# Kernel optimization log

Measured on AMD Instinct MI355X. Metric: run time of the kernel, lower is better.

Reference implementation:

```python
import jax, jax.numpy as jnp
import numpy as np

B, L, F = 16, 1024, 64
D = 256          # d_model (expand_factor=1 -> d_inner == d_model)
S = 2            # num_scales
N = 16           # state_size
H = 32           # fc hidden
EPS = 1e-5


def setup_inputs() -> dict:
    key = jax.random.key(0)
    ks = jax.random.split(key, 20)
    g = lambda i, shape, s=0.05: jax.random.normal(ks[i], shape, dtype=jnp.float32) * s
    return {
        "x": jax.random.normal(ks[0], (B, L, F), dtype=jnp.float32),
        "W_in": g(1, (F, D)), "b_in": jnp.zeros((D,), jnp.float32),
        # per-scale liquid-Mamba params, stacked over scales
        "Wd": g(2, (S, D, D)), "bd": jnp.zeros((S, D), jnp.float32),
        "WB": g(3, (S, D, N)), "WC": g(4, (S, D, N)),
        "Wtau": g(5, (S, D, D)),
        "A_log": jnp.broadcast_to(jnp.log(jnp.arange(1, N + 1, dtype=jnp.float32)), (S, D, N)).copy(),
        "Dp": jnp.ones((S, D), jnp.float32),
        "Wout": g(6, (S, D, D)),
        # head
        "ln_g": jnp.ones((D,), jnp.float32), "ln_b": jnp.zeros((D,), jnp.float32),
        "W1": g(7, (D, H)), "b1": jnp.zeros((H,), jnp.float32),
        "W2": g(8, (H, 1)), "b2": jnp.zeros((1,), jnp.float32),
    }


def _liquid_ssm(x, Wd, bd, WB, WC, Wtau, A_log, Dp, Wout):
    # x: [B,L,D] -> y: [B,L,D]. Selective scan with liquid time-constant gate.
    delta = jax.nn.softplus(jnp.einsum('bld,de->ble', x, Wd) + bd)   # [B,L,D]
    tau = jax.nn.sigmoid(jnp.einsum('bld,de->ble', x, Wtau))          # liquid gate
    delta = delta * tau
    Bm = jnp.einsum('bld,dn->bln', x, WB)                             # [B,L,N]
    Cm = jnp.einsum('bld,dn->bln', x, WC)                             # [B,L,N]
    A = -jnp.exp(A_log)                                               # [D,N]
    dA = jnp.exp(delta[..., None] * A)                                # [B,L,D,N]
    dBx = delta[..., None] * Bm[:, :, None, :] * x[..., None]         # [B,L,D,N]

    def step(h, inp):
        a_t, bx_t, c_t = inp                                          # [B,D,N],[B,D,N],[B,N]
        h = a_t * h + bx_t
        y = jnp.einsum('bdn,bn->bd', h, c_t)
        return h, y

    h0 = jnp.zeros((x.shape[0], x.shape[2], A.shape[1]), x.dtype)
    _, ys = jax.lax.scan(step, h0,
                         (dA.transpose(1, 0, 2, 3), dBx.transpose(1, 0, 2, 3), Cm.transpose(1, 0, 2)))
    y = ys.transpose(1, 0, 2) + x * Dp                                # skip connection
    return jnp.einsum('bld,de->ble', y, Wout)


def reference(x, W_in, b_in, Wd, bd, WB, WC, Wtau, A_log, Dp, Wout,
              ln_g, ln_b, W1, b1, W2, b2):
    h = jnp.einsum('blf,fd->bld', x, W_in) + b_in                     # input projection
    outs = [_liquid_ssm(h, Wd[s], bd[s], WB[s], WC[s], Wtau[s], A_log[s], Dp[s], Wout[s])
            for s in range(Wd.shape[0])]
    mamba_out = sum(outs) / len(outs)                                 # average over scales
    last = mamba_out[:, -1, :]                                        # [B,D]
    mu = jnp.mean(last, axis=-1, keepdims=True)
    var = jnp.var(last, axis=-1, keepdims=True)
    z = (last - mu) * jax.lax.rsqrt(var + EPS) * ln_g + ln_b          # LayerNorm
    z = jax.nn.relu(z @ W1 + b1)                                      # dropout is identity in eval
    return z @ W2 + b2                                                # [B,1]
```

## Files before the change

kernel.cpp:

```cpp
#include <hip/hip_runtime.h>
#include <hip/hip_bf16.h>
#include <math.h>

#define B_   16
#define L_   1024
#define F_   64
#define D_   256
#define S_   2
#define N_   16
#define H_   32
#define EPS_ 1e-5f
#define BL_  (B_*L_)
#define NCH_ 8
#define TC_  (L_/NCH_)
#define SUB_ 64
#define TSTR_ 68
#define LOG2E_ 1.44269504088896340736f
#define XBLK_ (BL_*F_/1024)

typedef __attribute__((ext_vector_type(8))) short  bf16x8;
typedef __attribute__((ext_vector_type(4))) float  f32x4;
typedef __attribute__((ext_vector_type(2))) float  f32x2;

typedef const __attribute__((address_space(1))) void* gas_ptr;
typedef __attribute__((address_space(3))) void*       las_ptr;

#if defined(__has_builtin)
# if __has_builtin(__builtin_amdgcn_exp2f)
#  define EXP2(x) __builtin_amdgcn_exp2f(x)
#  define ASCALE_ LOG2E_
# endif
#endif
#ifndef EXP2
# define EXP2(x) __expf(x)
# define ASCALE_ 1.0f
#endif

__device__ inline void async_copy16(const void* g, void* l) {
    __builtin_amdgcn_global_load_lds((gas_ptr)g, (las_ptr)l, 16, 0, 0);
}

__device__ inline unsigned short f2bf_rne(float x) {
    union { float f; unsigned u; } v; v.f = x;
    unsigned r = v.u + 0x7fff + ((v.u >> 16) & 1);
    return (unsigned short)(r >> 16);
}

__global__ __launch_bounds__(256) void k_prep(const float* __restrict__ x,
                                              const float* __restrict__ Win,
                                              const float* __restrict__ bin,
                                              const float* __restrict__ Wd,
                                              const float* __restrict__ bd,
                                              const float* __restrict__ Wt,
                                              const float* __restrict__ WB,
                                              unsigned short* __restrict__ x_hi,
                                              unsigned short* __restrict__ Weff_hi,
                                              float* __restrict__ bias_eff,
                                              unsigned short* __restrict__ WinT_hi,
                                              unsigned short* __restrict__ WBe_hi,
                                              float* __restrict__ bbias)
{
    const int blk = blockIdx.x;
    const int tid = threadIdx.x;

    if (blk < XBLK_) {
        const int i = (blk * 256 + tid) * 4;
        float4 v = *(const float4*)(x + i);
        ushort4 h4;
        h4.x = f2bf_rne(v.x);
        h4.y = f2bf_rne(v.y);
        h4.z = f2bf_rne(v.z);
        h4.w = f2bf_rne(v.w);
        *(ushort4*)(x_hi + i) = h4;
        return;
    }

    const int job4 = blk - XBLK_;
    const int j    = tid >> 6;
    const int f    = tid & 63;
    const int job  = job4 * 4 + j;

    __shared__ float col[4][D_];

    if (job < 1024) {
        const int s = job >> 9, n = job & 511;
        const float* W = (n < 256) ? (Wd + (size_t)s * D_ * D_) : (Wt + (size_t)s * D_ * D_);
        const int e = n & 255;
        for (int d = f; d < D_; d += 64) col[j][d] = W[(size_t)d * D_ + e];
        __syncthreads();
        float a = 0.f;
        for (int d = 0; d < D_; ++d) a += Win[(size_t)f * D_ + d] * col[j][d];
        Weff_hi[((size_t)s * 512 + n) * F_ + f] = f2bf_rne(a);
        if (f == 0) {
            float bb = 0.f;
            for (int d = 0; d < D_; ++d) bb += bin[d] * col[j][d];
            if (n < 256) bb += bd[s * D_ + e];
            bias_eff[s * 512 + n] = bb;
        }
    } else if (job < 1024 + D_) {
        const int d = job - 1024;
        WinT_hi[(size_t)d * F_ + f] = f2bf_rne(Win[(size_t)f * D_ + d]);
    } else {
        const int idx = job - (1024 + D_);
        const int s = idx >> 4, n = idx & 15;
        const float* wb = WB + (size_t)s * D_ * N_;
        float a = 0.f;
        for (int d = 0; d < D_; ++d) a += Win[(size_t)f * D_ + d] * wb[(size_t)d * N_ + n];
        WBe_hi[((size_t)s * N_ + n) * F_ + f] = f2bf_rne(a);
        if (f == 0) {
            float bb = 0.f;
            for (int d = 0; d < D_; ++d) bb += bin[d] * wb[(size_t)d * N_ + n];
            bbias[s * N_ + n] = bb;
        }
    }
}

__global__ __launch_bounds__(256) void k_fused_scan(
        const unsigned short* __restrict__ x_hi,
        const unsigned short* __restrict__ Weff_hi,
        const unsigned short* __restrict__ WinT_hi,
        const unsigned short* __restrict__ WBe_hi,
        const float* __restrict__ bias_eff,
        const float* __restrict__ bin,
        const float* __restrict__ bbias,
        const float* __restrict__ A_log,
        float* __restrict__ part,
        float* __restrict__ csum)
{
    const int dtile = blockIdx.x >> 3;
    const int c     = blockIdx.x & 7;
    const int b     = blockIdx.y;
    const int s     = blockIdx.z;
    const int d0    = dtile * 16;
    const int tid   = threadIdx.x;
    const int wid   = tid >> 6;
    const int lane  = tid & 63;
    const int l15   = lane & 15;
    const int quad  = lane >> 4;
    const int dl    = tid & 15;
    const int nl    = tid >> 4;

    __shared__ unsigned short Wh[64 * F_];
    __shared__ float sdl[16][TSTR_];
    __shared__ float sq [16][TSTR_];
    __shared__ float sb [16][TSTR_];

    const int r8 = lane >> 3;
    const int c8 = lane & 7;

    #pragma unroll
    for (int call = 0; call < 2; ++call) {
        const int rr = call * 8 + r8;
        const int ar = wid * 16 + rr;
        const int lc = (c8 - ar) & 7;
        const unsigned short* gh;
        if (wid == 0)      gh = Weff_hi + ((size_t)s * 512 + d0 + rr) * F_ + lc * 8;
        else if (wid == 1) gh = Weff_hi + ((size_t)s * 512 + 256 + d0 + rr) * F_ + lc * 8;
        else if (wid == 2) gh = WinT_hi + ((size_t)(d0 + rr)) * F_ + lc * 8;
        else               gh = WBe_hi + ((size_t)s * N_ + rr) * F_ + lc * 8;
        async_copy16(gh, &Wh[(wid * 16 + call * 8) * F_]);
    }

    const float bias_d = bias_eff[s * 512 + d0 + l15];
    const float bias_t = bias_eff[s * 512 + 256 + d0 + l15];
    const float bin_v  = bin[d0 + l15];
    const float bb_v   = bbias[s * N_ + l15];
    const float A2 = -__expf(A_log[((size_t)s * D_ + d0 + dl) * N_ + nl]) * ASCALE_;

    f32x2 st01 = {0.f, 0.f};
    f32x2 st23 = {0.f, 0.f};
    float As = 0.f;

    const int qoff = quad * 8;
    const int nsc  = TC_ / SUB_;

    bf16x8 fah0, fah1;
    {
        const size_t rowb = ((size_t)b * L_ + c * TC_ + (nsc - 1) * SUB_ + wid * 16 + l15) * F_;
        fah0 = *(const bf16x8*)(x_hi + rowb + qoff);
        fah1 = *(const bf16x8*)(x_hi + rowb + 32 + qoff);
    }
    __syncthreads();

    for (int sc = nsc - 1; sc >= 0; --sc) {
        f32x4 acc[4];
        #pragma unroll
        for (int g = 0; g < 4; ++g) acc[g] = (f32x4){0.f, 0.f, 0.f, 0.f};
        #pragma unroll
        for (int ks = 0; ks < 2; ++ks) {
            bf16x8 ah = ks ? fah1 : fah0;
            #pragma unroll
            for (int g = 0; g < 4; ++g) {
                const int brow = g * 16 + l15;
                const int pcB  = ((ks * 4 + quad) + brow) & 7;
                bf16x8 bh = *(const bf16x8*)&Wh[brow * F_ + pcB * 8];
                acc[g] = __builtin_amdgcn_mfma_f32_16x16x32_bf16(ah, bh, acc[g], 0, 0, 0);
            }
        }

        bf16x8 nah0, nah1;
        const bool more = (sc > 0);
        if (more) {
            const size_t rowb = ((size_t)b * L_ + c * TC_ + (sc - 1) * SUB_ + wid * 16 + l15) * F_;
            nah0 = *(const bf16x8*)(x_hi + rowb + qoff);
            nah1 = *(const bf16x8*)(x_hi + rowb + 32 + qoff);
        }

        __syncthreads();

        {
            f32x4 wd_, wq_, wb_;
            #pragma unroll
            for (int r = 0; r < 4; ++r) {
                const float pd  = acc[0][r] + bias_d;
                const float sp  = fmaxf(pd, 0.f) + __logf(1.f + __expf(-fabsf(pd)));
                const float sg  = 1.f / (1.f + __expf(-(acc[1][r] + bias_t)));
                const float dlt = sp * sg;
                const float hv  = acc[2][r] + bin_v;
                wd_[r] = dlt;
                wq_[r] = dlt * hv;
                wb_[r] = acc[3][r] + bb_v;
            }
            const int tcol = wid * 16 + quad * 4;
            *(f32x4*)&sdl[l15][tcol] = wd_;
            *(f32x4*)&sq [l15][tcol] = wq_;
            *(f32x4*)&sb [l15][tcol] = wb_;
        }
        __syncthreads();

        #pragma unroll 4
        for (int tt = SUB_ - 4; tt >= 0; tt -= 4) {
            f32x4 dp = *(const f32x4*)&sdl[dl][tt];
            f32x4 qp = *(const f32x4*)&sq [dl][tt];
            f32x4 bp = *(const f32x4*)&sb [nl][tt];
            const float a2v = fmaf(A2, dp.w, As);
            const float a1v = fmaf(A2, dp.z, a2v);
            const float a0v = fmaf(A2, dp.y, a1v);
            f32x2 e01, e23;
            e23.y = EXP2(As);
            e23.x = EXP2(a2v);
            e01.y = EXP2(a1v);
            e01.x = EXP2(a0v);
            f32x2 q01 = {qp.x, qp.y}, q23 = {qp.z, qp.w};
            f32x2 b01 = {bp.x, bp.y}, b23 = {bp.z, bp.w};
            st01 = q01 * b01 * e01 + st01;
            st23 = q23 * b23 * e23 + st23;
            As = fmaf(A2, dp.x, a0v);
        }

        if (more) { fah0 = nah0; fah1 = nah1; }
    }

    const size_t pb = ((size_t)s * B_ + b) * NCH_ + c;
    part[(pb * D_ + d0 + dl) * N_ + nl] = (st01.x + st01.y) + (st23.x + st23.y);
    if (nl == 0)
        csum[pb * D_ + d0 + dl] = As / A2;
}

__global__ __launch_bounds__(256) void k_ys(const float* __restrict__ x,
                                            const float* __restrict__ Win,
                                            const float* __restrict__ bin,
                                            const float* __restrict__ part,
                                            const float* __restrict__ csum,
                                            const float* __restrict__ A_log,
                                            const float* __restrict__ WC,
                                            const float* __restrict__ Dp,
                                            float* __restrict__ ys)
{
    const int s   = blockIdx.x;
    const int b   = blockIdx.y;
    const int tid = threadIdx.x;

    __shared__ float xr[F_];
    __shared__ float hl[D_];
    __shared__ float cm[N_];
    __shared__ float cred[N_][17];

    if (tid < F_) xr[tid] = x[((size_t)b * L_ + (L_ - 1)) * F_ + tid];
    __syncthreads();

    {
        float a = bin[tid];
        for (int f = 0; f < F_; ++f) a += xr[f] * Win[(size_t)f * D_ + tid];
        hl[tid] = a;
    }
    __syncthreads();

    {
        const int n  = tid & 15;
        const int dq = tid >> 4;
        float a = 0.f;
        for (int d = dq * 16; d < dq * 16 + 16; ++d)
            a += hl[d] * WC[((size_t)s * D_ + d) * N_ + n];
        cred[n][dq] = a;
    }
    __syncthreads();
    if (tid < N_) {
        float a = 0.f;
        #pragma unroll
        for (int q = 0; q < 16; ++q) a += cred[tid][q];
        cm[tid] = a;
    }
    __syncthreads();

    const float* al = A_log + ((size_t)s * D_ + tid) * N_;
    float a2v[N_];
    #pragma unroll
    for (int n = 0; n < N_; ++n) a2v[n] = -__expf(al[n]);
    const size_t cbase = ((size_t)s * B_ + b) * NCH_;
    float acc = 0.f;
    float tail = 0.f;
    for (int c = NCH_ - 1; c >= 0; --c) {
        const float* pp = part + ((cbase + c) * D_ + tid) * N_;
        #pragma unroll
        for (int n = 0; n < N_; ++n)
            acc += cm[n] * __expf(a2v[n] * tail) * pp[n];
        tail += csum[(cbase + c) * D_ + tid];
    }
    ys[((size_t)s * B_ + b) * D_ + tid] = acc + hl[tid] * Dp[s * D_ + tid];
}

__global__ __launch_bounds__(256) void k_last(const float* __restrict__ ys,
                                              const float* __restrict__ Wout,
                                              float* __restrict__ last)
{
    const int b  = blockIdx.x;
    const int e0 = blockIdx.y * 64;
    const int tid = threadIdx.x;
    const int e  = tid & 63;
    const int kq = tid >> 6;

    __shared__ float ysl[S_ * D_];
    __shared__ float red[4][64];

    #pragma unroll
    for (int j = tid; j < S_ * D_; j += 256) {
        const int ss = j >> 8, dd = j & 255;
        ysl[j] = ys[((size_t)ss * B_ + b) * D_ + dd];
    }
    __syncthreads();

    float a = 0.f;
    for (int k = kq * 128; k < kq * 128 + 128; ++k) {
        const int ss = k >> 8, dd = k & 255;
        a += ysl[k] * Wout[((size_t)ss * D_ + dd) * D_ + e0 + e];
    }
    red[kq][e] = a;
    __syncthreads();
    if (kq == 0) {
        const float v = (red[0][e] + red[1][e] + red[2][e] + red[3][e]) * (1.f / S_);
        last[(size_t)b * D_ + e0 + e] = v;
    }
}

__global__ __launch_bounds__(256) void k_head(const float* __restrict__ last,
                                              const float* __restrict__ ln_g,
                                              const float* __restrict__ ln_b,
                                              const float* __restrict__ W1,
                                              const float* __restrict__ b1,
                                              const float* __restrict__ W2,
                                              const float* __restrict__ b2,
                                              float* __restrict__ out)
{
    const int b   = blockIdx.x;
    const int tid = threadIdx.x;

    __shared__ float zv[D_];
    __shared__ float red1[256];
    __shared__ float red2[256];
    __shared__ float r1[H_];

    const float v = last[(size_t)b * D_ + tid];
    red1[tid] = v;
    red2[tid] = v * v;
    __syncthreads();
    for (int off = 128; off > 0; off >>= 1) {
        if (tid < off) { red1[tid] += red1[tid + off]; red2[tid] += red2[tid + off]; }
        __syncthreads();
    }
    const float mu  = red1[0] * (1.f / D_);
    const float var = red2[0] * (1.f / D_) - mu * mu;
    const float z = (v - mu) * rsqrtf(var + EPS_) * ln_g[tid] + ln_b[tid];
    zv[tid] = z;
    __syncthreads();

    if (tid < H_) {
        float a = b1[tid];
        for (int e = 0; e < D_; ++e) a += zv[e] * W1[(size_t)e * H_ + tid];
        r1[tid] = fmaxf(a, 0.f);
    }
    __syncthreads();
    if (tid == 0) {
        float a = b2[0];
        for (int j = 0; j < H_; ++j) a += r1[j] * W2[j];
        out[b] = a;
    }
}

extern "C" void kernel_launch(void* const* d_in, const int* in_sizes, int n_in,
                              void* d_out, int out_size, void* d_ws, size_t ws_size,
                              hipStream_t stream)
{
    const float* x     = (const float*)d_in[0];
    const float* Win   = (const float*)d_in[1];
    const float* bin   = (const float*)d_in[2];
    const float* Wd    = (const float*)d_in[3];
    const float* bd    = (const float*)d_in[4];
    const float* WB    = (const float*)d_in[5];
    const float* WC    = (const float*)d_in[6];
    const float* Wtau  = (const float*)d_in[7];
    const float* A_log = (const float*)d_in[8];
    const float* Dp    = (const float*)d_in[9];
    const float* Wout  = (const float*)d_in[10];
    const float* ln_g  = (const float*)d_in[11];
    const float* ln_b  = (const float*)d_in[12];
    const float* W1    = (const float*)d_in[13];
    const float* b1    = (const float*)d_in[14];
    const float* W2    = (const float*)d_in[15];
    const float* b2    = (const float*)d_in[16];
    float* out = (float*)d_out;

    char* ws = (char*)d_ws;
    const size_t MB = 1024 * 1024;
    const size_t KB = 1024;
    unsigned short* x_hi     = (unsigned short*)(ws);
    unsigned short* Weff_hi  = (unsigned short*)(ws + 2 * MB);
    unsigned short* WinT_hi  = (unsigned short*)(ws + 2 * MB + 128 * KB);
    unsigned short* WBe_hi   = (unsigned short*)(ws + 2 * MB + 160 * KB);
    float*          bias_eff = (float*)(ws + 2 * MB + 164 * KB);
    float*          bbias    = (float*)(ws + 2 * MB + 168 * KB);
    float*          part     = (float*)(ws + 3 * MB);
    float*          csum     = (float*)(ws + 7 * MB);
    float*          ysbuf    = (float*)(ws + 7 * MB + 256 * KB);
    float*          lastbuf  = (float*)(ws + 7 * MB + 288 * KB);

    hipLaunchKernelGGL(k_prep, dim3(XBLK_ + 328), dim3(256), 0, stream,
                       x, Win, bin, Wd, bd, Wtau, WB,
                       x_hi, Weff_hi, bias_eff, WinT_hi, WBe_hi, bbias);
    hipLaunchKernelGGL(k_fused_scan, dim3((D_ / 16) * NCH_, B_, S_), dim3(256), 0, stream,
                       x_hi, Weff_hi, WinT_hi, WBe_hi,
                       bias_eff, bin, bbias, A_log, part, csum);
    hipLaunchKernelGGL(k_ys,   dim3(S_, B_), dim3(256), 0, stream,
                       x, Win, bin, part, csum, A_log, WC, Dp, ysbuf);
    hipLaunchKernelGGL(k_last, dim3(B_, 4), dim3(256), 0, stream, ysbuf, Wout, lastbuf);
    hipLaunchKernelGGL(k_head, dim3(B_), dim3(256), 0, stream,
                       lastbuf, ln_g, ln_b, W1, b1, W2, b2, out);
}
```

Baseline: 162.1 us.

## Double scan chunks to one tile each and fuse tail kernels into one

Doubles the number of sequence chunks in the fused scan so each block handles a single 64-step tile, dropping the inner sub-chunk loop, the prefetch and one barrier per tile while launching twice as many blocks. The three small epilogue kernels (chunk combine, output projection, head) are merged into a single per-batch kernel to remove two launches and their intermediate global buffers. The cost is twice the partial-state traffic and a longer serial chunk combine, and the fused tail runs on only 16 blocks, each doing the full Wout matvec serially per thread.

```diff
diff --git a/kernel.cpp b/kernel.cpp
--- a/kernel.cpp
+++ b/kernel.cpp
@@ -11,9 +11,8 @@
 #define H_   32
 #define EPS_ 1e-5f
 #define BL_  (B_*L_)
-#define NCH_ 8
+#define NCH_ 16
 #define TC_  (L_/NCH_)
-#define SUB_ 64
 #define TSTR_ 68
 #define LOG2E_ 1.44269504088896340736f
 #define XBLK_ (BL_*F_/1024)
@@ -127,8 +126,8 @@
         float* __restrict__ part,
         float* __restrict__ csum)
 {
-    const int dtile = blockIdx.x >> 3;
-    const int c     = blockIdx.x & 7;
+    const int dtile = blockIdx.x >> 4;
+    const int c     = blockIdx.x & 15;
     const int b     = blockIdx.y;
     const int s     = blockIdx.z;
     const int d0    = dtile * 16;
@@ -167,88 +166,71 @@
     const float bb_v   = bbias[s * N_ + l15];
     const float A2 = -__expf(A_log[((size_t)s * D_ + d0 + dl) * N_ + nl]) * ASCALE_;
 
+    const int qoff = quad * 8;
+    bf16x8 fah0, fah1;
+    {
+        const size_t rowb = ((size_t)b * L_ + c * TC_ + wid * 16 + l15) * F_;
+        fah0 = *(const bf16x8*)(x_hi + rowb + qoff);
+        fah1 = *(const bf16x8*)(x_hi + rowb + 32 + qoff);
+    }
+    __syncthreads();
+
+    f32x4 acc[4];
+    #pragma unroll
+    for (int g = 0; g < 4; ++g) acc[g] = (f32x4){0.f, 0.f, 0.f, 0.f};
+    #pragma unroll
+    for (int ks = 0; ks < 2; ++ks) {
+        bf16x8 ah = ks ? fah1 : fah0;
+        #pragma unroll
+        for (int g = 0; g < 4; ++g) {
+            const int brow = g * 16 + l15;
+            const int pcB  = ((ks * 4 + quad) + brow) & 7;
+            bf16x8 bh = *(const bf16x8*)&Wh[brow * F_ + pcB * 8];
+            acc[g] = __builtin_amdgcn_mfma_f32_16x16x32_bf16(ah, bh, acc[g], 0, 0, 0);
+        }
+    }
+
+    {
+        f32x4 wd_, wq_, wb_;
+        #pragma unroll
+        for (int r = 0; r < 4; ++r) {
+            const float pd  = acc[0][r] + bias_d;
+            const float sp  = fmaxf(pd, 0.f) + __logf(1.f + __expf(-fabsf(pd)));
+            const float sg  = 1.f / (1.f + __expf(-(acc[1][r] + bias_t)));
+            const float dlt = sp * sg;
+            const float hv  = acc[2][r] + bin_v;
+            wd_[r] = dlt;
+            wq_[r] = dlt * hv;
+            wb_[r] = acc[3][r] + bb_v;
+        }
+        const int tcol = wid * 16 + quad * 4;
+        *(f32x4*)&sdl[l15][tcol] = wd_;
+        *(f32x4*)&sq [l15][tcol] = wq_;
+        *(f32x4*)&sb [l15][tcol] = wb_;
+    }
+    __syncthreads();
+
     f32x2 st01 = {0.f, 0.f};
     f32x2 st23 = {0.f, 0.f};
     float As = 0.f;
-
-    const int qoff = quad * 8;
-    const int nsc  = TC_ / SUB_;
-
-    bf16x8 fah0, fah1;
-    {
-        const size_t rowb = ((size_t)b * L_ + c * TC_ + (nsc - 1) * SUB_ + wid * 16 + l15) * F_;
-        fah0 = *(const bf16x8*)(x_hi + rowb + qoff);
-        fah1 = *(const bf16x8*)(x_hi + rowb + 32 + qoff);
-    }
-    __syncthreads();
-
-    for (int sc = nsc - 1; sc >= 0; --sc) {
-        f32x4 acc[4];
-        #pragma unroll
-        for (int g = 0; g < 4; ++g) acc[g] = (f32x4){0.f, 0.f, 0.f, 0.f};
-        #pragma unroll
-        for (int ks = 0; ks < 2; ++ks) {
-            bf16x8 ah = ks ? fah1 : fah0;
-            #pragma unroll
-            for (int g = 0; g < 4; ++g) {
-                const int brow = g * 16 + l15;
-                const int pcB  = ((ks * 4 + quad) + brow) & 7;
-                bf16x8 bh = *(const bf16x8*)&Wh[brow * F_ + pcB * 8];
-                acc[g] = __builtin_amdgcn_mfma_f32_16x16x32_bf16(ah, bh, acc[g], 0, 0, 0);
-            }
-        }
-
-        bf16x8 nah0, nah1;
-        const bool more = (sc > 0);
-        if (more) {
-            const size_t rowb = ((size_t)b * L_ + c * TC_ + (sc - 1) * SUB_ + wid * 16 + l15) * F_;
-            nah0 = *(const bf16x8*)(x_hi + rowb + qoff);
-            nah1 = *(const bf16x8*)(x_hi + rowb + 32 + qoff);
-        }
-
-        __syncthreads();
-
-        {
-            f32x4 wd_, wq_, wb_;
-            #pragma unroll
-            for (int r = 0; r < 4; ++r) {
-                const float pd  = acc[0][r] + bias_d;
-                const float sp  = fmaxf(pd, 0.f) + __logf(1.f + __expf(-fabsf(pd)));
-                const float sg  = 1.f / (1.f + __expf(-(acc[1][r] + bias_t)));
-                const float dlt = sp * sg;
-                const float hv  = acc[2][r] + bin_v;
-                wd_[r] = dlt;
-                wq_[r] = dlt * hv;
-                wb_[r] = acc[3][r] + bb_v;
-            }
-            const int tcol = wid * 16 + quad * 4;
-            *(f32x4*)&sdl[l15][tcol] = wd_;
-            *(f32x4*)&sq [l15][tcol] = wq_;
-            *(f32x4*)&sb [l15][tcol] = wb_;
-        }
-        __syncthreads();
-
-        #pragma unroll 4
-        for (int tt = SUB_ - 4; tt >= 0; tt -= 4) {
-            f32x4 dp = *(const f32x4*)&sdl[dl][tt];
-            f32x4 qp = *(const f32x4*)&sq [dl][tt];
-            f32x4 bp = *(const f32x4*)&sb [nl][tt];
-            const float a2v = fmaf(A2, dp.w, As);
-            const float a1v = fmaf(A2, dp.z, a2v);
-            const float a0v = fmaf(A2, dp.y, a1v);
-            f32x2 e01, e23;
-            e23.y = EXP2(As);
-            e23.x = EXP2(a2v);
-            e01.y = EXP2(a1v);
-            e01.x = EXP2(a0v);
-            f32x2 q01 = {qp.x, qp.y}, q23 = {qp.z, qp.w};
-            f32x2 b01 = {bp.x, bp.y}, b23 = {bp.z, bp.w};
-            st01 = q01 * b01 * e01 + st01;
-            st23 = q23 * b23 * e23 + st23;
-            As = fmaf(A2, dp.x, a0v);
-        }
-
-        if (more) { fah0 = nah0; fah1 = nah1; }
+    #pragma unroll 4
+    for (int tt = TC_ - 4; tt >= 0; tt -= 4) {
+        f32x4 dp = *(const f32x4*)&sdl[dl][tt];
+        f32x4 qp = *(const f32x4*)&sq [dl][tt];
+        f32x4 bp = *(const f32x4*)&sb [nl][tt];
+        const float a2v = fmaf(A2, dp.w, As);
+        const float a1v = fmaf(A2, dp.z, a2v);
+        const float a0v = fmaf(A2, dp.y, a1v);
+        f32x2 e01, e23;
+        e23.y = EXP2(As);
+        e23.x = EXP2(a2v);
+        e01.y = EXP2(a1v);
+        e01.x = EXP2(a0v);
+        f32x2 q01 = {qp.x, qp.y}, q23 = {qp.z, qp.w};
+        f32x2 b01 = {bp.x, bp.y}, b23 = {bp.z, bp.w};
+        st01 = q01 * b01 * e01 + st01;
+        st23 = q23 * b23 * e23 + st23;
+        As = fmaf(A2, dp.x, a0v);
     }
 
     const size_t pb = ((size_t)s * B_ + b) * NCH_ + c;
@@ -257,103 +239,15 @@
         csum[pb * D_ + d0 + dl] = As / A2;
 }
 
-__global__ __launch_bounds__(256) void k_ys(const float* __restrict__ x,
-                                            const float* __restrict__ Win,
-                                            const float* __restrict__ bin,
-                                            const float* __restrict__ part,
-                                            const float* __restrict__ csum,
-                                            const float* __restrict__ A_log,
-                                            const float* __restrict__ WC,
-                                            const float* __restrict__ Dp,
-                                            float* __restrict__ ys)
-{
-    const int s   = blockIdx.x;
-    const int b   = blockIdx.y;
-    const int tid = threadIdx.x;
-
-    __shared__ float xr[F_];
-    __shared__ float hl[D_];
-    __shared__ float cm[N_];
-    __shared__ float cred[N_][17];
-
-    if (tid < F_) xr[tid] = x[((size_t)b * L_ + (L_ - 1)) * F_ + tid];
-    __syncthreads();
-
-    {
-        float a = bin[tid];
-        for (int f = 0; f < F_; ++f) a += xr[f] * Win[(size_t)f * D_ + tid];
-        hl[tid] = a;
-    }
-    __syncthreads();
-
-    {
-        const int n  = tid & 15;
-        const int dq = tid >> 4;
-        float a = 0.f;
-        for (int d = dq * 16; d < dq * 16 + 16; ++d)
-            a += hl[d] * WC[((size_t)s * D_ + d) * N_ + n];
-        cred[n][dq] = a;
-    }
-    __syncthreads();
-    if (tid < N_) {
-        float a = 0.f;
-        #pragma unroll
-        for (int q = 0; q < 16; ++q) a += cred[tid][q];
-        cm[tid] = a;
-    }
-    __syncthreads();
-
-    const float* al = A_log + ((size_t)s * D_ + tid) * N_;
-    float a2v[N_];
-    #pragma unroll
-    for (int n = 0; n < N_; ++n) a2v[n] = -__expf(al[n]);
-    const size_t cbase = ((size_t)s * B_ + b) * NCH_;
-    float acc = 0.f;
-    float tail = 0.f;
-    for (int c = NCH_ - 1; c >= 0; --c) {
-        const float* pp = part + ((cbase + c) * D_ + tid) * N_;
-        #pragma unroll
-        for (int n = 0; n < N_; ++n)
-            acc += cm[n] * __expf(a2v[n] * tail) * pp[n];
-        tail += csum[(cbase + c) * D_ + tid];
-    }
-    ys[((size_t)s * B_ + b) * D_ + tid] = acc + hl[tid] * Dp[s * D_ + tid];
-}
-
-__global__ __launch_bounds__(256) void k_last(const float* __restrict__ ys,
+__global__ __launch_bounds__(256) void k_tail(const float* __restrict__ x,
+                                              const float* __restrict__ Win,
+                                              const float* __restrict__ bin,
+                                              const float* __restrict__ part,
+                                              const float* __restrict__ csum,
+                                              const float* __restrict__ A_log,
+                                              const float* __restrict__ WC,
+                                              const float* __restrict__ Dp,
                                               const float* __restrict__ Wout,
-                                              float* __restrict__ last)
-{
-    const int b  = blockIdx.x;
-    const int e0 = blockIdx.y * 64;
-    const int tid = threadIdx.x;
-    const int e  = tid & 63;
-    const int kq = tid >> 6;
-
-    __shared__ float ysl[S_ * D_];
-    __shared__ float red[4][64];
-
-    #pragma unroll
-    for (int j = tid; j < S_ * D_; j += 256) {
-        const int ss = j >> 8, dd = j & 255;
-        ysl[j] = ys[((size_t)ss * B_ + b) * D_ + dd];
-    }
-    __syncthreads();
-
-    float a = 0.f;
-    for (int k = kq * 128; k < kq * 128 + 128; ++k) {
-        const int ss = k >> 8, dd = k & 255;
-        a += ysl[k] * Wout[((size_t)ss * D_ + dd) * D_ + e0 + e];
-    }
-    red[kq][e] = a;
-    __syncthreads();
-    if (kq == 0) {
-        const float v = (red[0][e] + red[1][e] + red[2][e] + red[3][e]) * (1.f / S_);
-        last[(size_t)b * D_ + e0 + e] = v;
-    }
-}
-
-__global__ __launch_bounds__(256) void k_head(const float* __restrict__ last,
                                               const float* __restrict__ ln_g,
                                               const float* __restrict__ ln_b,
                                               const float* __restrict__ W1,
@@ -365,12 +259,73 @@
     const int b   = blockIdx.x;
     const int tid = threadIdx.x;
 
+    __shared__ float xr[F_];
+    __shared__ float hl[D_];
+    __shared__ float cm[S_][N_];
+    __shared__ float cred[N_][17];
+    __shared__ float ysl[S_][D_];
     __shared__ float zv[D_];
     __shared__ float red1[256];
     __shared__ float red2[256];
     __shared__ float r1[H_];
 
-    const float v = last[(size_t)b * D_ + tid];
+    if (tid < F_) xr[tid] = x[((size_t)b * L_ + (L_ - 1)) * F_ + tid];
+    __syncthreads();
+
+    {
+        float a = bin[tid];
+        for (int f = 0; f < F_; ++f) a += xr[f] * Win[(size_t)f * D_ + tid];
+        hl[tid] = a;
+    }
+    __syncthreads();
+
+    for (int s = 0; s < S_; ++s) {
+        const int n  = tid & 15;
+        const int dq = tid >> 4;
+        float a = 0.f;
+        for (int d = dq * 16; d < dq * 16 + 16; ++d)
+            a += hl[d] * WC[((size_t)s * D_ + d) * N_ + n];
+        cred[n][dq] = a;
+        __syncthreads();
+        if (tid < N_) {
+            float acc = 0.f;
+            #pragma unroll
+            for (int q = 0; q < 16; ++q) acc += cred[tid][q];
+            cm[s][tid] = acc;
+        }
+        __syncthreads();
+    }
+
+    for (int s = 0; s < S_; ++s) {
+        const float* al = A_log + ((size_t)s * D_ + tid) * N_;
+        float a2v[N_];
+        #pragma unroll
+        for (int n = 0; n < N_; ++n) a2v[n] = -__expf(al[n]);
+        const size_t cbase = ((size_t)s * B_ + b) * NCH_;
+        float acc = 0.f;
+        float tail = 0.f;
+        for (int c = NCH_ - 1; c >= 0; --c) {
+            const float* pp = part + ((cbase + c) * D_ + tid) * N_;
+            #pragma unroll
+            for (int n = 0; n < N_; ++n)
+                acc += cm[s][n] * __expf(a2v[n] * tail) * pp[n];
+            tail += csum[(cbase + c) * D_ + tid];
+        }
+        ysl[s][tid] = acc + hl[tid] * Dp[s * D_ + tid];
+    }
+    __syncthreads();
+
+    float v;
+    {
+        float a = 0.f;
+        #pragma unroll 2
+        for (int s = 0; s < S_; ++s) {
+            const float* wo = Wout + (size_t)s * D_ * D_;
+            for (int d = 0; d < D_; ++d) a += ysl[s][d] * wo[(size_t)d * D_ + tid];
+        }
+        v = a * (1.f / S_);
+    }
+
     red1[tid] = v;
     red2[tid] = v * v;
     __syncthreads();
@@ -430,9 +385,7 @@
     float*          bias_eff = (float*)(ws + 2 * MB + 164 * KB);
     float*          bbias    = (float*)(ws + 2 * MB + 168 * KB);
     float*          part     = (float*)(ws + 3 * MB);
-    float*          csum     = (float*)(ws + 7 * MB);
-    float*          ysbuf    = (float*)(ws + 7 * MB + 256 * KB);
-    float*          lastbuf  = (float*)(ws + 7 * MB + 288 * KB);
+    float*          csum     = (float*)(ws + 11 * MB);
 
     hipLaunchKernelGGL(k_prep, dim3(XBLK_ + 328), dim3(256), 0, stream,
                        x, Win, bin, Wd, bd, Wtau, WB,
@@ -440,9 +393,7 @@
     hipLaunchKernelGGL(k_fused_scan, dim3((D_ / 16) * NCH_, B_, S_), dim3(256), 0, stream,
                        x_hi, Weff_hi, WinT_hi, WBe_hi,
                        bias_eff, bin, bbias, A_log, part, csum);
-    hipLaunchKernelGGL(k_ys,   dim3(S_, B_), dim3(256), 0, stream,
-                       x, Win, bin, part, csum, A_log, WC, Dp, ysbuf);
-    hipLaunchKernelGGL(k_last, dim3(B_, 4), dim3(256), 0, stream, ysbuf, Wout, lastbuf);
-    hipLaunchKernelGGL(k_head, dim3(B_), dim3(256), 0, stream,
-                       lastbuf, ln_g, ln_b, W1, b1, W2, b2, out);
-}
+    hipLaunchKernelGGL(k_tail, dim3(B_), dim3(256), 0, stream,
+                       x, Win, bin, part, csum, A_log, WC, Dp, Wout,
+                       ln_g, ln_b, W1, b1, W2, b2, out);
+}
```

New measurement: 180.0 us. 1.11x slower.

## Double scan chunk count and parallelize chunk combine over d-tiles

Applied to the files above, without the earlier changes.

Splits the sequence into 16 chunks of 64 steps instead of 8 chunks of 128, so each scan block does one MFMA projection and one 64-step scan with no inner sub-chunk loop or prefetch. This doubles the grid of the fused scan kernel (more blocks to fill the CUs, shorter serial chain per block). The combine kernel k_ys is re-gridded over 16-wide d tiles, with each thread handling one (d,n) pair plus a shared-memory reduction, so the longer chunk carry runs in parallel. The cost is twice the partial-state traffic, and the combine kernel now recomputes its input projection in every d-tile block.

```diff
diff --git a/kernel.cpp b/kernel.cpp
--- a/kernel.cpp
+++ b/kernel.cpp
@@ -11,9 +11,8 @@
 #define H_   32
 #define EPS_ 1e-5f
 #define BL_  (B_*L_)
-#define NCH_ 8
+#define NCH_ 16
 #define TC_  (L_/NCH_)
-#define SUB_ 64
 #define TSTR_ 68
 #define LOG2E_ 1.44269504088896340736f
 #define XBLK_ (BL_*F_/1024)
@@ -127,8 +126,8 @@
         float* __restrict__ part,
         float* __restrict__ csum)
 {
-    const int dtile = blockIdx.x >> 3;
-    const int c     = blockIdx.x & 7;
+    const int dtile = blockIdx.x >> 4;
+    const int c     = blockIdx.x & 15;
     const int b     = blockIdx.y;
     const int s     = blockIdx.z;
     const int d0    = dtile * 16;
@@ -167,88 +166,71 @@
     const float bb_v   = bbias[s * N_ + l15];
     const float A2 = -__expf(A_log[((size_t)s * D_ + d0 + dl) * N_ + nl]) * ASCALE_;
 
+    const int qoff = quad * 8;
+    bf16x8 fah0, fah1;
+    {
+        const size_t rowb = ((size_t)b * L_ + c * TC_ + wid * 16 + l15) * F_;
+        fah0 = *(const bf16x8*)(x_hi + rowb + qoff);
+        fah1 = *(const bf16x8*)(x_hi + rowb + 32 + qoff);
+    }
+    __syncthreads();
+
+    f32x4 acc[4];
+    #pragma unroll
+    for (int g = 0; g < 4; ++g) acc[g] = (f32x4){0.f, 0.f, 0.f, 0.f};
+    #pragma unroll
+    for (int ks = 0; ks < 2; ++ks) {
+        bf16x8 ah = ks ? fah1 : fah0;
+        #pragma unroll
+        for (int g = 0; g < 4; ++g) {
+            const int brow = g * 16 + l15;
+            const int pcB  = ((ks * 4 + quad) + brow) & 7;
+            bf16x8 bh = *(const bf16x8*)&Wh[brow * F_ + pcB * 8];
+            acc[g] = __builtin_amdgcn_mfma_f32_16x16x32_bf16(ah, bh, acc[g], 0, 0, 0);
+        }
+    }
+
+    {
+        f32x4 wd_, wq_, wb_;
+        #pragma unroll
+        for (int r = 0; r < 4; ++r) {
+            const float pd  = acc[0][r] + bias_d;
+            const float sp  = fmaxf(pd, 0.f) + __logf(1.f + __expf(-fabsf(pd)));
+            const float sg  = 1.f / (1.f + __expf(-(acc[1][r] + bias_t)));
+            const float dlt = sp * sg;
+            const float hv  = acc[2][r] + bin_v;
+            wd_[r] = dlt;
+            wq_[r] = dlt * hv;
+            wb_[r] = acc[3][r] + bb_v;
+        }
+        const int tcol = wid * 16 + quad * 4;
+        *(f32x4*)&sdl[l15][tcol] = wd_;
+        *(f32x4*)&sq [l15][tcol] = wq_;
+        *(f32x4*)&sb [l15][tcol] = wb_;
+    }
+    __syncthreads();
+
     f32x2 st01 = {0.f, 0.f};
     f32x2 st23 = {0.f, 0.f};
     float As = 0.f;
-
-    const int qoff = quad * 8;
-    const int nsc  = TC_ / SUB_;
-
-    bf16x8 fah0, fah1;
-    {
-        const size_t rowb = ((size_t)b * L_ + c * TC_ + (nsc - 1) * SUB_ + wid * 16 + l15) * F_;
-        fah0 = *(const bf16x8*)(x_hi + rowb + qoff);
-        fah1 = *(const bf16x8*)(x_hi + rowb + 32 + qoff);
-    }
-    __syncthreads();
-
-    for (int sc = nsc - 1; sc >= 0; --sc) {
-        f32x4 acc[4];
-        #pragma unroll
-        for (int g = 0; g < 4; ++g) acc[g] = (f32x4){0.f, 0.f, 0.f, 0.f};
-        #pragma unroll
-        for (int ks = 0; ks < 2; ++ks) {
-            bf16x8 ah = ks ? fah1 : fah0;
-            #pragma unroll
-            for (int g = 0; g < 4; ++g) {
-                const int brow = g * 16 + l15;
-                const int pcB  = ((ks * 4 + quad) + brow) & 7;
-                bf16x8 bh = *(const bf16x8*)&Wh[brow * F_ + pcB * 8];
-                acc[g] = __builtin_amdgcn_mfma_f32_16x16x32_bf16(ah, bh, acc[g], 0, 0, 0);
-            }
-        }
-
-        bf16x8 nah0, nah1;
-        const bool more = (sc > 0);
-        if (more) {
-            const size_t rowb = ((size_t)b * L_ + c * TC_ + (sc - 1) * SUB_ + wid * 16 + l15) * F_;
-            nah0 = *(const bf16x8*)(x_hi + rowb + qoff);
-            nah1 = *(const bf16x8*)(x_hi + rowb + 32 + qoff);
-        }
-
-        __syncthreads();
-
-        {
-            f32x4 wd_, wq_, wb_;
-            #pragma unroll
-            for (int r = 0; r < 4; ++r) {
-                const float pd  = acc[0][r] + bias_d;
-                const float sp  = fmaxf(pd, 0.f) + __logf(1.f + __expf(-fabsf(pd)));
-                const float sg  = 1.f / (1.f + __expf(-(acc[1][r] + bias_t)));
-                const float dlt = sp * sg;
-                const float hv  = acc[2][r] + bin_v;
-                wd_[r] = dlt;
-                wq_[r] = dlt * hv;
-                wb_[r] = acc[3][r] + bb_v;
-            }
-            const int tcol = wid * 16 + quad * 4;
-            *(f32x4*)&sdl[l15][tcol] = wd_;
-            *(f32x4*)&sq [l15][tcol] = wq_;
-            *(f32x4*)&sb [l15][tcol] = wb_;
-        }
-        __syncthreads();
-
-        #pragma unroll 4
-        for (int tt = SUB_ - 4; tt >= 0; tt -= 4) {
-            f32x4 dp = *(const f32x4*)&sdl[dl][tt];
-            f32x4 qp = *(const f32x4*)&sq [dl][tt];
-            f32x4 bp = *(const f32x4*)&sb [nl][tt];
-            const float a2v = fmaf(A2, dp.w, As);
-            const float a1v = fmaf(A2, dp.z, a2v);
-            const float a0v = fmaf(A2, dp.y, a1v);
-            f32x2 e01, e23;
-            e23.y = EXP2(As);
-            e23.x = EXP2(a2v);
-            e01.y = EXP2(a1v);
-            e01.x = EXP2(a0v);
-            f32x2 q01 = {qp.x, qp.y}, q23 = {qp.z, qp.w};
-            f32x2 b01 = {bp.x, bp.y}, b23 = {bp.z, bp.w};
-            st01 = q01 * b01 * e01 + st01;
-            st23 = q23 * b23 * e23 + st23;
-            As = fmaf(A2, dp.x, a0v);
-        }
-
-        if (more) { fah0 = nah0; fah1 = nah1; }
+    #pragma unroll 4
+    for (int tt = TC_ - 4; tt >= 0; tt -= 4) {
+        f32x4 dp = *(const f32x4*)&sdl[dl][tt];
+        f32x4 qp = *(const f32x4*)&sq [dl][tt];
+        f32x4 bp = *(const f32x4*)&sb [nl][tt];
+        const float a2v = fmaf(A2, dp.w, As);
+        const float a1v = fmaf(A2, dp.z, a2v);
+        const float a0v = fmaf(A2, dp.y, a1v);
+        f32x2 e01, e23;
+        e23.y = EXP2(As);
+        e23.x = EXP2(a2v);
+        e01.y = EXP2(a1v);
+        e01.x = EXP2(a0v);
+        f32x2 q01 = {qp.x, qp.y}, q23 = {qp.z, qp.w};
+        f32x2 b01 = {bp.x, bp.y}, b23 = {bp.z, bp.w};
+        st01 = q01 * b01 * e01 + st01;
+        st23 = q23 * b23 * e23 + st23;
+        As = fmaf(A2, dp.x, a0v);
     }
 
     const size_t pb = ((size_t)s * B_ + b) * NCH_ + c;
@@ -269,12 +251,18 @@
 {
     const int s   = blockIdx.x;
     const int b   = blockIdx.y;
+    const int d0  = blockIdx.z * 16;
     const int tid = threadIdx.x;
+    const int dl  = tid & 15;
+    const int nl  = tid >> 4;
+    const int d   = d0 + dl;
 
     __shared__ float xr[F_];
     __shared__ float hl[D_];
+    __shared__ float cred[N_][17];
     __shared__ float cm[N_];
-    __shared__ float cred[N_][17];
+    __shared__ float csh[NCH_][16];
+    __shared__ float red[N_][17];
 
     if (tid < F_) xr[tid] = x[((size_t)b * L_ + (L_ - 1)) * F_ + tid];
     __syncthreads();
@@ -290,9 +278,11 @@
         const int n  = tid & 15;
         const int dq = tid >> 4;
         float a = 0.f;
-        for (int d = dq * 16; d < dq * 16 + 16; ++d)
-            a += hl[d] * WC[((size_t)s * D_ + d) * N_ + n];
+        for (int dd = dq * 16; dd < dq * 16 + 16; ++dd)
+            a += hl[dd] * WC[((size_t)s * D_ + dd) * N_ + n];
         cred[n][dq] = a;
+        const size_t cbase0 = ((size_t)s * B_ + b) * NCH_;
+        csh[tid >> 4][tid & 15] = csum[(cbase0 + (tid >> 4)) * D_ + d0 + (tid & 15)];
     }
     __syncthreads();
     if (tid < N_) {
@@ -303,21 +293,26 @@
     }
     __syncthreads();
 
-    const float* al = A_log + ((size_t)s * D_ + tid) * N_;
-    float a2v[N_];
-    #pragma unroll
-    for (int n = 0; n < N_; ++n) a2v[n] = -__expf(al[n]);
+    const float A = -__expf(A_log[((size_t)s * D_ + d) * N_ + nl]);
     const size_t cbase = ((size_t)s * B_ + b) * NCH_;
     float acc = 0.f;
     float tail = 0.f;
+    #pragma unroll
     for (int c = NCH_ - 1; c >= 0; --c) {
-        const float* pp = part + ((cbase + c) * D_ + tid) * N_;
+        const float p = part[((cbase + c) * D_ + d) * N_ + nl];
+        acc += __expf(A * tail) * p;
+        tail += csh[c][dl];
+    }
+    red[nl][dl] = cm[nl] * acc;
+    __syncthreads();
+
+    if (tid < 16) {
+        float a = 0.f;
         #pragma unroll
-        for (int n = 0; n < N_; ++n)
-            acc += cm[n] * __expf(a2v[n] * tail) * pp[n];
-        tail += csum[(cbase + c) * D_ + tid];
-    }
-    ys[((size_t)s * B_ + b) * D_ + tid] = acc + hl[tid] * Dp[s * D_ + tid];
+        for (int n = 0; n < N_; ++n) a += red[n][tid];
+        const int dd = d0 + tid;
+        ys[((size_t)s * B_ + b) * D_ + dd] = a + hl[dd] * Dp[s * D_ + dd];
+    }
 }
 
 __global__ __launch_bounds__(256) void k_last(const float* __restrict__ ys,
@@ -430,9 +425,9 @@
     float*          bias_eff = (float*)(ws + 2 * MB + 164 * KB);
     float*          bbias    = (float*)(ws + 2 * MB + 168 * KB);
     float*          part     = (float*)(ws + 3 * MB);
-    float*          csum     = (float*)(ws + 7 * MB);
-    float*          ysbuf    = (float*)(ws + 7 * MB + 256 * KB);
-    float*          lastbuf  = (float*)(ws + 7 * MB + 288 * KB);
+    float*          csum     = (float*)(ws + 11 * MB);
+    float*          ysbuf    = (float*)(ws + 11 * MB + 512 * KB);
+    float*          lastbuf  = (float*)(ws + 11 * MB + 544 * KB);
 
     hipLaunchKernelGGL(k_prep, dim3(XBLK_ + 328), dim3(256), 0, stream,
                        x, Win, bin, Wd, bd, Wtau, WB,
@@ -440,7 +435,7 @@
     hipLaunchKernelGGL(k_fused_scan, dim3((D_ / 16) * NCH_, B_, S_), dim3(256), 0, stream,
                        x_hi, Weff_hi, WinT_hi, WBe_hi,
                        bias_eff, bin, bbias, A_log, part, csum);
-    hipLaunchKernelGGL(k_ys,   dim3(S_, B_), dim3(256), 0, stream,
+    hipLaunchKernelGGL(k_ys,   dim3(S_, B_, D_ / 16), dim3(256), 0, stream,
                        x, Win, bin, part, csum, A_log, WC, Dp, ysbuf);
     hipLaunchKernelGGL(k_last, dim3(B_, 4), dim3(256), 0, stream, ysbuf, Wout, lastbuf);
     hipLaunchKernelGGL(k_head, dim3(B_), dim3(256), 0, stream,
```

New measurement: 161.6 us. No clear change (-0.3%).
